# Kernel optimization log

Measured on AMD Instinct MI355X. Metric: run time of the kernel, lower is better.

Reference implementation:

```python
import jax, jax.numpy as jnp
import numpy as np

B, S, H = 1, 2048, 4096
NQ, NKV, HD = 32, 8, 128
BLOCK = 128            # block size of block_streaming_attn_func
SINK_BLOCKS = 1        # sink_size 128 / BLOCK
LOCAL_BLOCKS = 8       # local_window_size 1024 / BLOCK
ROPE_BASE = 10000.0


def setup_inputs() -> dict:
    key = jax.random.key(0)
    ks = jax.random.split(key, 5)
    s = 0.02
    return {
        "hidden_states": jax.random.normal(ks[0], (B, S, H), jnp.float32),
        "wq": jax.random.normal(ks[1], (H, NQ * HD), jnp.float32) * s,
        "wk": jax.random.normal(ks[2], (H, NKV * HD), jnp.float32) * s,
        "wv": jax.random.normal(ks[3], (H, NKV * HD), jnp.float32) * s,
        "wo": jax.random.normal(ks[4], (NQ * HD, H), jnp.float32) * s,
    }


def _rope(x):
    # x: [B, S, heads, HD]; non-interleaved (GPT-NeoX half-split) rotary, full head_dim
    pos = jnp.arange(S, dtype=jnp.float32)
    inv = 1.0 / (ROPE_BASE ** (jnp.arange(0, HD, 2, dtype=jnp.float32) / HD))
    f = pos[:, None] * inv[None, :]                 # [S, HD/2]
    cos = jnp.cos(f)[None, :, None, :]
    sin = jnp.sin(f)[None, :, None, :]
    x1, x2 = x[..., : HD // 2], x[..., HD // 2 :]
    return jnp.concatenate([x1 * cos - x2 * sin, x2 * cos + x1 * sin], axis=-1).astype(x.dtype)


def _streaming_mask():
    # causal + (sink blocks OR local window blocks), block granularity = BLOCK
    idx = jnp.arange(S)
    blk = idx // BLOCK
    causal = idx[None, :] <= idx[:, None]
    sink = blk[None, :] < SINK_BLOCKS
    local = (blk[:, None] - blk[None, :]) < LOCAL_BLOCKS
    return causal & (sink | local)                  # [S, S]


def reference(hidden_states, wq, wk, wv, wo):
    q = (hidden_states @ wq).reshape(B, S, NQ, HD)
    k = (hidden_states @ wk).reshape(B, S, NKV, HD)
    v = (hidden_states @ wv).reshape(B, S, NKV, HD)
    q = _rope(q)
    k = _rope(k)
    rep = NQ // NKV                                 # repeat_kv (GQA)
    k = jnp.repeat(k, rep, axis=2)
    v = jnp.repeat(v, rep, axis=2)
    scores = jnp.einsum('bqhd,bkhd->bhqk', q, k) / jnp.sqrt(jnp.float32(HD))
    mask = _streaming_mask()
    scores = jnp.where(mask[None, None], scores, jnp.finfo(scores.dtype).min)
    p = jax.nn.softmax(scores, axis=-1)
    out = jnp.einsum('bhqk,bkhd->bqhd', p, v).reshape(B, S, NQ * HD)
    return out @ wo
```

## Files before the change

kernel.cpp:

```cpp
#include <hip/hip_runtime.h>
#include <hip/hip_bf16.h>
#include <math.h>

typedef __bf16 bf16;
typedef __attribute__((ext_vector_type(8))) __bf16 bf16x8;
typedef __attribute__((ext_vector_type(4))) __bf16 bf16x4;
typedef __attribute__((ext_vector_type(4))) float f32x4;

#define MFMA16(a, b, c) __builtin_amdgcn_mfma_f32_16x16x32_bf16(a, b, c, 0, 0, 0)

__device__ __forceinline__ void load16_lds(const bf16* g, bf16* l) {
  __builtin_amdgcn_global_load_lds(
      (const __attribute__((address_space(1))) void*)g,
      (__attribute__((address_space(3))) void*)l, 16, 0, 0);
}

__global__ __launch_bounds__(256) void cast_k(const float* __restrict__ src,
                                              bf16* __restrict__ dst) {
  const size_t i = ((size_t)blockIdx.x * 256 + threadIdx.x) * 8;
  f32x4 a = *(const f32x4*)(src + i);
  f32x4 b = *(const f32x4*)(src + i + 4);
  bf16x8 h;
#pragma unroll
  for (int j = 0; j < 4; ++j) {
    h[j] = (bf16)a[j];
    h[4 + j] = (bf16)b[j];
  }
  *(bf16x8*)(dst + i) = h;
}

__global__ __launch_bounds__(256) void transpose_cast_k(
    const float* __restrict__ src, bf16* __restrict__ dst, int rows,
    int cols) {
  __shared__ float tile[64][65];
  const int c0 = blockIdx.x * 64, r0 = blockIdx.y * 64;
  const int tid = threadIdx.x;
  const int lr = tid >> 4;
  const int lc = (tid & 15) * 4;
#pragma unroll
  for (int i = 0; i < 4; ++i) {
    const int row = lr + i * 16;
    const f32x4 v = *(const f32x4*)&src[(size_t)(r0 + row) * cols + c0 + lc];
#pragma unroll
    for (int j = 0; j < 4; ++j) tile[row][lc + j] = v[j];
  }
  __syncthreads();
#pragma unroll
  for (int i = 0; i < 4; ++i) {
    const int orow = lr + i * 16;
    bf16x4 h;
#pragma unroll
    for (int j = 0; j < 4; ++j) h[j] = (bf16)tile[lc + j][orow];
    *(bf16x4*)&dst[(size_t)(c0 + orow) * rows + r0 + lc] = h;
  }
}

#define BARX() __builtin_amdgcn_s_barrier()
#define LGKM0() asm volatile("s_waitcnt lgkmcnt(0)" ::: "memory")
#define VMC0() asm volatile("s_waitcnt vmcnt(0)" ::: "memory")
#define VMCN()                                           \
  {                                                      \
    if constexpr (NFRAG == 3) {                          \
      asm volatile("s_waitcnt vmcnt(3)" ::: "memory");   \
    } else {                                             \
      asm volatile("s_waitcnt vmcnt(2)" ::: "memory");   \
    }                                                    \
  }

#define DS_A(BUF, QM)                                                       \
  {                                                                         \
    _Pragma("unroll") for (int mi = 0; mi < 4; ++mi)                        \
        _Pragma("unroll") for (int kk = 0; kk < 2; ++kk)                    \
            a[mi][kk] = *(const bf16x8*)&As[BUF][(aBase ^ (kk << 5)) +      \
                                                (QM)*4096 + mi * 1024];     \
  }

#define DS_B(BUF)                                                           \
  {                                                                         \
    _Pragma("unroll") for (int ni = 0; ni < NFRAG; ++ni)                    \
        _Pragma("unroll") for (int kk = 0; kk < 2; ++kk)                    \
            b[ni][kk] = *(const bf16x8*)&Bs[BUF][(bBase ^ (kk << 5)) +      \
                                                 ni * 1024];                \
  }

#define MMAC(QM)                                                            \
  {                                                                         \
    __builtin_amdgcn_s_setprio(1);                                          \
    _Pragma("unroll") for (int mi = 0; mi < 4; ++mi)                        \
        _Pragma("unroll") for (int ni = 0; ni < NFRAG; ++ni) {              \
      acc[(QM)*4 + mi][ni] = MFMA16(a[mi][0], b[ni][0], acc[(QM)*4 + mi][ni]); \
      acc[(QM)*4 + mi][ni] = MFMA16(a[mi][1], b[ni][1], acc[(QM)*4 + mi][ni]); \
    }                                                                       \
    __builtin_amdgcn_s_setprio(0);                                          \
  }

#define STAGE_A(BUF, T)                                                     \
  {                                                                         \
    const bf16* g0 = aS0 + (size_t)(T)*64;                                  \
    const bf16* g1 = aS1 + (size_t)(T)*64;                                  \
    bf16* l = &As[BUF][w * 512];                                            \
    load16_lds(g0, l);                                                      \
    load16_lds(g1, l + 4096);                                               \
    load16_lds(g0 + ROWK128, l + 8192);                                     \
    load16_lds(g1 + ROWK128, l + 12288);                                    \
  }

#define STAGE_B(BUF, T)                                                     \
  {                                                                         \
    _Pragma("unroll") for (int jj = 0; jj < NFRAG; ++jj)                    \
        load16_lds(bS0 + (size_t)(T)*64 + (size_t)jj * 64 * K,              \
                   &Bs[BUF][jj * 4096 + w * 512]);                          \
  }

template <typename OT, int NFRAG, int EPI>
__global__ __launch_bounds__(512, 2) void gemm256(
    const bf16* __restrict__ A, const bf16* __restrict__ Bt,
    OT* __restrict__ C, bf16* __restrict__ Ck, bf16* __restrict__ Cv, int K,
    int ldc) {
  constexpr int BN = NFRAG * 64;
  const size_t ROWK128 = (size_t)128 * K;
  __shared__ bf16 As[2][256 * 64];
  __shared__ bf16 Bs[2][BN * 64];

  const int tid = threadIdx.x;
  const int lane = tid & 63;
  const int w = tid >> 6;
  const int wm = w >> 2;
  const int wn = w & 3;
  const int quad = lane >> 4;
  const int m16 = lane & 15;

  const int rowBase = blockIdx.y * 256;
  const int colBase = blockIdx.x * BN;

  const int u0 = tid, u1 = 512 + tid;
  const int r0 = u0 >> 3, c0s = (u0 & 7) ^ (r0 & 7);
  const int r1 = u1 >> 3, c1s = (u1 & 7) ^ (r1 & 7);
  const bf16* aS0 = A + (size_t)(rowBase + r0) * K + c0s * 8;
  const bf16* aS1 = A + (size_t)(rowBase + r1) * K + c1s * 8;
  const bf16* bS0 = Bt + (size_t)(colBase + r0) * K + c0s * 8;

  const int xsw = (m16 & 7) << 3;
  const int ko0 = (quad * 8) ^ xsw;
  const int aBase = (wm * 128 + m16) * 64 + ko0;
  const int bBase = (wn * (16 * NFRAG) + m16) * 64 + ko0;

  f32x4 acc[8][NFRAG];
#pragma unroll
  for (int i = 0; i < 8; ++i)
#pragma unroll
    for (int j = 0; j < NFRAG; ++j) acc[i][j] = (f32x4){0.f, 0.f, 0.f, 0.f};

  bf16x8 a[4][2], b[NFRAG][2];

  STAGE_B(0, 0);
  STAGE_A(0, 0);
  STAGE_B(1, 1);
  VMCN();
  BARX();

  const int nT = K / 64;
#pragma unroll 1
  for (int j = 0; j < nT / 2; ++j) {
    const int pO1 = 2 * j + 1;
    const int pE = (2 * j + 2 < nT) ? 2 * j + 2 : 0;
    const int pO2 = (2 * j + 3 < nT) ? 2 * j + 3 : 0;
    DS_B(0);
    DS_A(0, 0);
    STAGE_A(1, pO1);
    LGKM0();
    MMAC(0);
    BARX();
    DS_A(0, 1);
    STAGE_B(0, pE);
    VMCN();
    LGKM0();
    MMAC(1);
    BARX();
    DS_B(1);
    DS_A(1, 0);
    STAGE_A(0, pE);
    LGKM0();
    MMAC(0);
    BARX();
    DS_A(1, 1);
    STAGE_B(1, pO2);
    VMCN();
    LGKM0();
    MMAC(1);
    BARX();
  }
  VMC0();

#pragma unroll
  for (int am = 0; am < 8; ++am) {
    const int gr0 = rowBase + wm * 128 + am * 16 + quad * 4;
#pragma unroll
    for (int an = 0; an < NFRAG; ++an) {
      const int base16 = colBase + wn * (16 * NFRAG) + an * 16;
      const int gc = base16 + m16;
      if constexpr (EPI == 0) {
#pragma unroll
        for (int r = 0; r < 4; ++r)
          C[(size_t)(gr0 + r) * ldc + gc] = (OT)acc[am][an][r];
      } else {
        if (base16 < 4096) {
#pragma unroll
          for (int r = 0; r < 4; ++r)
            C[(size_t)(gr0 + r) * 4096 + gc] = (OT)acc[am][an][r];
        } else if (base16 < 5120) {
#pragma unroll
          for (int r = 0; r < 4; ++r)
            Ck[(size_t)(gr0 + r) * 1024 + (gc - 4096)] = (bf16)acc[am][an][r];
        } else {
          bf16x4 h;
#pragma unroll
          for (int r = 0; r < 4; ++r) h[r] = (bf16)acc[am][an][r];
          *(bf16x4*)&Cv[(size_t)(gc - 5120) * 2048 + gr0] = h;
        }
      }
    }
  }
}

__global__ __launch_bounds__(256) void rope_k(bf16* __restrict__ qb,
                                              bf16* __restrict__ kb) {
  const int NQTOT = 2048 * 32 * 64;
  const int NKTOT = 2048 * 8 * 64;
  int idx = blockIdx.x * 256 + threadIdx.x;
  bf16* buf;
  int nh, rest;
  if (idx < NQTOT) {
    buf = qb;
    nh = 32;
    rest = idx;
  } else {
    rest = idx - NQTOT;
    if (rest >= NKTOT) return;
    buf = kb;
    nh = 8;
  }
  const int j = rest & 63;
  const int hs = rest >> 6;
  const int hh = hs % nh;
  const int s = hs / nh;
  const float inv = __expf((float)j * -0.14391157f);
  const float f = (float)s * inv;
  float sn, cs;
  __sincosf(f, &sn, &cs);
  const size_t base = (size_t)(s * nh + hh) * 128 + j;
  const float x1 = (float)buf[base];
  const float x2 = (float)buf[base + 64];
  buf[base] = (bf16)(x1 * cs - x2 * sn);
  buf[base + 64] = (bf16)(x2 * cs + x1 * sn);
}

__global__ __launch_bounds__(256, 2) void attn_k(const bf16* __restrict__ q,
                                                 const bf16* __restrict__ kbuf,
                                                 const bf16* __restrict__ vT,
                                                 bf16* __restrict__ attn) {
  const int qb = 15 - blockIdx.x;
  const int h = blockIdx.y;
  const int kvh = h >> 2;
  const int tid = threadIdx.x;
  const int lane = tid & 63;
  const int w = tid >> 6;
  const int quad = lane >> 4;
  const int m16 = lane & 15;

  __shared__ bf16 Ks[4][64 * 32];
  __shared__ bf16 Vs[2][128 * 32];
  __shared__ bf16 Ps[128][72];

  const int qrow0 = qb * 128 + w * 32;

  bf16x8 qf[2][4];
#pragma unroll
  for (int rt = 0; rt < 2; ++rt)
#pragma unroll
    for (int kt = 0; kt < 4; ++kt)
      qf[rt][kt] = *(const bf16x8*)&q[(size_t)(qrow0 + rt * 16 + m16) * 4096 +
                                      h * 128 + kt * 32 + quad * 8];

  f32x4 o[2][8];
  float lsum[2][4];
#pragma unroll
  for (int rt = 0; rt < 2; ++rt) {
#pragma unroll
    for (int dt = 0; dt < 8; ++dt) o[rt][dt] = (f32x4){0.f, 0.f, 0.f, 0.f};
#pragma unroll
    for (int r = 0; r < 4; ++r) lsum[rt][r] = 0.f;
  }

  const float scale = 0.08838834764831845f;
  const bf16* kbase = kbuf + kvh * 128;
  const bf16* vbase = vT + (size_t)(kvh * 128) * 2048;

  const int klocal = (lane >> 2);
  const int kseg = (lane & 3) * 8;

  for (int b = 0; b <= qb; ++b) {
    if (b > 0 && (qb - b) >= 8) continue;
    const bool diag = (b == qb);
    for (int half = 0; half < 2; ++half) {
      const int gk0 = b * 128 + half * 64;

#pragma unroll
      for (int i = 0; i < 4; ++i) {
        const int j = w * 4 + i;
        const int kt = j >> 2, grp = (j & 3) * 16;
        load16_lds(kbase + (size_t)(gk0 + grp + klocal) * 1024 + kt * 32 + kseg,
                   &Ks[kt][grp * 32]);
      }
#pragma unroll
      for (int i = 0; i < 4; ++i) {
        const int j = w * 4 + i;
        const int kc = j >> 3, grp = (j & 7) * 16;
        load16_lds(vbase + (size_t)(grp + klocal) * 2048 + gk0 + kc * 32 + kseg,
                   &Vs[kc][grp * 32]);
      }
      __syncthreads();

      const bool skip = diag && (half * 64 > w * 32 + 31);
      if (!skip) {
        f32x4 sc[2][4];
#pragma unroll
        for (int rt = 0; rt < 2; ++rt)
#pragma unroll
          for (int ct = 0; ct < 4; ++ct)
            sc[rt][ct] = (f32x4){0.f, 0.f, 0.f, 0.f};
#pragma unroll
        for (int kt = 0; kt < 4; ++kt) {
          bf16x8 kf[4];
#pragma unroll
          for (int ct = 0; ct < 4; ++ct)
            kf[ct] = *(const bf16x8*)&Ks[kt][(ct * 16 + m16) * 32 + quad * 8];
#pragma unroll
          for (int rt = 0; rt < 2; ++rt)
#pragma unroll
            for (int ct = 0; ct < 4; ++ct)
              sc[rt][ct] = MFMA16(qf[rt][kt], kf[ct], sc[rt][ct]);
        }

#pragma unroll
        for (int rt = 0; rt < 2; ++rt)
#pragma unroll
          for (int ct = 0; ct < 4; ++ct)
#pragma unroll
            for (int r = 0; r < 4; ++r) {
              float p = __expf(sc[rt][ct][r] * scale);
              if (diag) {
                const int colg = gk0 + ct * 16 + m16;
                const int rowg = qrow0 + rt * 16 + quad * 4 + r;
                if (colg > rowg) p = 0.f;
              }
              lsum[rt][r] += p;
              Ps[w * 32 + rt * 16 + quad * 4 + r][ct * 16 + m16] = (bf16)p;
            }

#pragma unroll
        for (int rt = 0; rt < 2; ++rt)
#pragma unroll
          for (int kc = 0; kc < 2; ++kc) {
            const bf16x8 pa =
                *(const bf16x8*)&Ps[w * 32 + rt * 16 + m16][kc * 32 + quad * 8];
#pragma unroll
            for (int dt = 0; dt < 8; ++dt) {
              const bf16x8 vb =
                  *(const bf16x8*)&Vs[kc][(dt * 16 + m16) * 32 + quad * 8];
              o[rt][dt] = MFMA16(pa, vb, o[rt][dt]);
            }
          }
      }
      __syncthreads();
    }
  }

#pragma unroll
  for (int rt = 0; rt < 2; ++rt) {
    float inv[4];
#pragma unroll
    for (int r = 0; r < 4; ++r) {
      float s = lsum[rt][r];
      s += __shfl_xor(s, 1);
      s += __shfl_xor(s, 2);
      s += __shfl_xor(s, 4);
      s += __shfl_xor(s, 8);
      inv[r] = 1.0f / s;
    }
#pragma unroll
    for (int dt = 0; dt < 8; ++dt)
#pragma unroll
      for (int r = 0; r < 4; ++r)
        attn[(size_t)(qrow0 + rt * 16 + quad * 4 + r) * 4096 + h * 128 +
             dt * 16 + m16] = (bf16)(o[rt][dt][r] * inv[r]);
  }
}

extern "C" void kernel_launch(void* const* d_in, const int* in_sizes, int n_in,
                              void* d_out, int out_size, void* d_ws,
                              size_t ws_size, hipStream_t stream) {
  const float* hidden = (const float*)d_in[0];
  const float* wq = (const float*)d_in[1];
  const float* wk = (const float*)d_in[2];
  const float* wv = (const float*)d_in[3];
  const float* wo = (const float*)d_in[4];
  float* out = (float*)d_out;

  const size_t MB = 1024 * 1024;
  bf16* hiddenB = (bf16*)d_ws;
  bf16* wqkvT = (bf16*)((char*)d_ws + 16 * MB);
  bf16* woT = (bf16*)d_ws;
  bf16* attnb = (bf16*)((char*)d_ws + 32 * MB);
  bf16* qbuf = (bf16*)((char*)d_ws + 64 * MB);
  bf16* kbuf = (bf16*)((char*)d_ws + 80 * MB);
  bf16* vT = (bf16*)((char*)d_ws + 84 * MB);

  cast_k<<<4096, 256, 0, stream>>>(hidden, hiddenB);
  transpose_cast_k<<<dim3(64, 64), 256, 0, stream>>>(wq, wqkvT, 4096, 4096);
  transpose_cast_k<<<dim3(16, 64), 256, 0, stream>>>(
      wk, wqkvT + (size_t)4096 * 4096, 4096, 1024);
  transpose_cast_k<<<dim3(16, 64), 256, 0, stream>>>(
      wv, wqkvT + (size_t)5120 * 4096, 4096, 1024);

  gemm256<bf16, 3, 2><<<dim3(32, 8), 512, 0, stream>>>(hiddenB, wqkvT, qbuf,
                                                       kbuf, vT, 4096, 4096);

  rope_k<<<(2048 * 32 * 64 + 2048 * 8 * 64) / 256, 256, 0, stream>>>(qbuf,
                                                                     kbuf);

  transpose_cast_k<<<dim3(64, 64), 256, 0, stream>>>(wo, woT, 4096, 4096);

  attn_k<<<dim3(16, 32), 256, 0, stream>>>(qbuf, kbuf, vT, attnb);

  gemm256<float, 2, 0><<<dim3(32, 8), 512, 0, stream>>>(
      attnb, woT, out, nullptr, nullptr, 4096, 4096);
}
```

Baseline: 436.6 us.

## Double-buffer GEMM register fragments and deepen global-to-LDS prefetch

Restructures the projection GEMM main loop so that LDS fragment reads for the next quarter-step happen after the current MFMA batch is issued, using separate a0/a1 and bC/bN register sets. Both K tiles are prefetched in the prologue and the A staging is split into halves, which keeps more global loads in flight (the vmcnt thresholds rise accordingly). The aim is to hide LDS and global latency behind MFMA work. In exchange it uses more VGPRs, which could hurt occupancy at 512 threads with 2 blocks per CU, and the barrier ordering becomes harder to verify as race-free.

Result: faster. 422.8 us (-3.2%).

```diff
diff --git a/kernel.cpp b/kernel.cpp
--- a/kernel.cpp
+++ b/kernel.cpp
@@ -61,47 +61,62 @@
 #define VMCN()                                           \
   {                                                      \
     if constexpr (NFRAG == 3) {                          \
-      asm volatile("s_waitcnt vmcnt(3)" ::: "memory");   \
+      asm volatile("s_waitcnt vmcnt(7)" ::: "memory");   \
     } else {                                             \
-      asm volatile("s_waitcnt vmcnt(2)" ::: "memory");   \
+      asm volatile("s_waitcnt vmcnt(6)" ::: "memory");   \
     }                                                    \
   }
 
-#define DS_A(BUF, QM)                                                       \
+#define DS_A0(BUF, DST)                                                     \
   {                                                                         \
     _Pragma("unroll") for (int mi = 0; mi < 4; ++mi)                        \
         _Pragma("unroll") for (int kk = 0; kk < 2; ++kk)                    \
-            a[mi][kk] = *(const bf16x8*)&As[BUF][(aBase ^ (kk << 5)) +      \
-                                                (QM)*4096 + mi * 1024];     \
-  }
-
-#define DS_B(BUF)                                                           \
+            DST[mi][kk] =                                                   \
+                *(const bf16x8*)&As[BUF][(aBase ^ (kk << 5)) + mi * 1024];  \
+  }
+
+#define DS_A1(BUF, DST)                                                     \
+  {                                                                         \
+    _Pragma("unroll") for (int mi = 0; mi < 4; ++mi)                        \
+        _Pragma("unroll") for (int kk = 0; kk < 2; ++kk)                    \
+            DST[mi][kk] = *(const bf16x8*)&As[BUF][(aBase ^ (kk << 5)) +    \
+                                                   4096 + mi * 1024];       \
+  }
+
+#define DS_B(BUF, DST)                                                      \
   {                                                                         \
     _Pragma("unroll") for (int ni = 0; ni < NFRAG; ++ni)                    \
         _Pragma("unroll") for (int kk = 0; kk < 2; ++kk)                    \
-            b[ni][kk] = *(const bf16x8*)&Bs[BUF][(bBase ^ (kk << 5)) +      \
-                                                 ni * 1024];                \
-  }
-
-#define MMAC(QM)                                                            \
+            DST[ni][kk] = *(const bf16x8*)&Bs[BUF][(bBase ^ (kk << 5)) +    \
+                                                   ni * 1024];              \
+  }
+
+#define MMAC(QM, AR, BR)                                                    \
   {                                                                         \
     __builtin_amdgcn_s_setprio(1);                                          \
     _Pragma("unroll") for (int mi = 0; mi < 4; ++mi)                        \
         _Pragma("unroll") for (int ni = 0; ni < NFRAG; ++ni) {              \
-      acc[(QM)*4 + mi][ni] = MFMA16(a[mi][0], b[ni][0], acc[(QM)*4 + mi][ni]); \
-      acc[(QM)*4 + mi][ni] = MFMA16(a[mi][1], b[ni][1], acc[(QM)*4 + mi][ni]); \
+      acc[(QM)*4 + mi][ni] =                                                \
+          MFMA16(AR[mi][0], BR[ni][0], acc[(QM)*4 + mi][ni]);               \
+      acc[(QM)*4 + mi][ni] =                                                \
+          MFMA16(AR[mi][1], BR[ni][1], acc[(QM)*4 + mi][ni]);               \
     }                                                                       \
     __builtin_amdgcn_s_setprio(0);                                          \
   }
 
-#define STAGE_A(BUF, T)                                                     \
+#define STAGE_A0(BUF, T)                                                    \
   {                                                                         \
     const bf16* g0 = aS0 + (size_t)(T)*64;                                  \
+    bf16* l = &As[BUF][w * 512];                                            \
+    load16_lds(g0, l);                                                      \
+    load16_lds(g0 + ROWK128, l + 8192);                                     \
+  }
+
+#define STAGE_A1(BUF, T)                                                    \
+  {                                                                         \
     const bf16* g1 = aS1 + (size_t)(T)*64;                                  \
     bf16* l = &As[BUF][w * 512];                                            \
-    load16_lds(g0, l);                                                      \
     load16_lds(g1, l + 4096);                                               \
-    load16_lds(g0 + ROWK128, l + 8192);                                     \
     load16_lds(g1 + ROWK128, l + 12288);                                    \
   }
 
@@ -151,43 +166,53 @@
 #pragma unroll
     for (int j = 0; j < NFRAG; ++j) acc[i][j] = (f32x4){0.f, 0.f, 0.f, 0.f};
 
-  bf16x8 a[4][2], b[NFRAG][2];
+  bf16x8 a0[4][2], a1[4][2], bC[NFRAG][2], bN[NFRAG][2];
 
   STAGE_B(0, 0);
-  STAGE_A(0, 0);
+  STAGE_A0(0, 0);
+  STAGE_A1(0, 0);
   STAGE_B(1, 1);
+  STAGE_A0(1, 1);
+  STAGE_A1(1, 1);
   VMCN();
+  BARX();
+  DS_B(0, bC);
+  DS_A0(0, a0);
+  LGKM0();
   BARX();
 
   const int nT = K / 64;
 #pragma unroll 1
   for (int j = 0; j < nT / 2; ++j) {
-    const int pO1 = 2 * j + 1;
-    const int pE = (2 * j + 2 < nT) ? 2 * j + 2 : 0;
-    const int pO2 = (2 * j + 3 < nT) ? 2 * j + 3 : 0;
-    DS_B(0);
-    DS_A(0, 0);
-    STAGE_A(1, pO1);
+    const int pe2 = (2 * j + 2 < nT) ? 2 * j + 2 : 0;
+    const int po2 = (2 * j + 3 < nT) ? 2 * j + 3 : 0;
+    MMAC(0, a0, bC);
+    VMCN();
+    DS_A1(0, a1);
+    STAGE_B(0, pe2);
+    STAGE_A0(0, pe2);
     LGKM0();
-    MMAC(0);
     BARX();
-    DS_A(0, 1);
-    STAGE_B(0, pE);
+    MMAC(1, a1, bC);
     VMCN();
+    DS_B(1, bN);
+    DS_A0(1, a0);
+    STAGE_A1(0, pe2);
     LGKM0();
-    MMAC(1);
     BARX();
-    DS_B(1);
-    DS_A(1, 0);
-    STAGE_A(0, pE);
+    MMAC(0, a0, bN);
+    VMCN();
+    DS_A1(1, a1);
+    STAGE_B(1, po2);
+    STAGE_A0(1, po2);
     LGKM0();
-    MMAC(0);
     BARX();
-    DS_A(1, 1);
-    STAGE_B(1, pO2);
+    MMAC(1, a1, bN);
     VMCN();
+    DS_B(0, bC);
+    DS_A0(0, a0);
+    STAGE_A1(1, po2);
     LGKM0();
-    MMAC(1);
     BARX();
   }
   VMC0();
```
